# Optimization experiments

Measured on AMD Instinct MI355X. Metric: run time of the kernel, lower is better.

The kernel has to match this reference:

```python
import jax, jax.numpy as jnp
import numpy as np

N_NODES = 50000
N_EDGES = 800000
IN_CH = 64
OUT_CH = 64
EDGE_DIM = 3


def setup_inputs() -> dict:
    key = jax.random.key(0)
    k1, k2, k3, k4, k5 = jax.random.split(key, 5)
    x = jax.random.normal(k1, (N_NODES, IN_CH), dtype=jnp.float32)
    edge_index = jax.random.randint(k2, (2, N_EDGES), 0, N_NODES, dtype=jnp.int64)
    edge_attr = jax.random.normal(k3, (N_EDGES, EDGE_DIM), dtype=jnp.float32)
    # nn.Linear default init: U(-1/sqrt(fan_in), 1/sqrt(fan_in)); weight shape [out, in]
    bound = 1.0 / np.sqrt(IN_CH)
    phi_w = jax.random.uniform(k4, (OUT_CH, IN_CH), minval=-bound, maxval=bound, dtype=jnp.float32)
    psi_w = jax.random.uniform(k5, (OUT_CH, IN_CH), minval=-bound, maxval=bound, dtype=jnp.float32)
    return {"x": x, "edge_index": edge_index, "edge_attr": edge_attr, "phi_w": phi_w, "psi_w": psi_w}


def reference(x, edge_index, edge_attr, phi_w, psi_w):
    src, dst = edge_index[0], edge_index[1]
    # gather -> linear -> scale by edge-attr L2 norm
    msg = jnp.einsum('ei,oi->eo', x[src], phi_w)  # [E, out_ch]
    msg = msg * jnp.linalg.norm(edge_attr, axis=1, keepdims=True)
    # scatter-add into destination nodes
    agg = jax.ops.segment_sum(msg, dst, num_segments=x.shape[0])  # [N, out_ch]
    return jnp.einsum('ni,oi->no', x, psi_w) + agg
```

## Files before the change

kernel.cpp:

```cpp
#include <hip/hip_runtime.h>
#include <math.h>

#define NN 50000
#define NE 800000
#define CH 64
#define CSLOT 64
#define LDA 129

typedef float v4f __attribute__((ext_vector_type(4)));
typedef unsigned short u16x8 __attribute__((ext_vector_type(8)));

__device__ __forceinline__ unsigned short f2bf(float f) {
    unsigned int u = __float_as_uint(f);
    unsigned int r = (u + 0x7FFFu + ((u >> 16) & 1u)) >> 16;
    return (unsigned short)r;
}
__device__ __forceinline__ float bf2f(unsigned short h) {
    return __uint_as_float(((unsigned int)h) << 16);
}

__global__ __launch_bounds__(256) void cvt_k(const float* __restrict__ x,
                                             unsigned short* __restrict__ x16) {
    const int i = blockIdx.x * 256 + threadIdx.x;
    if (i * 8 >= NN * CH) return;
    const v4f a = *(const v4f*)(x + (size_t)i * 8);
    const v4f b = *(const v4f*)(x + (size_t)i * 8 + 4);
    u16x8 o;
    o[0] = f2bf(a.x); o[1] = f2bf(a.y); o[2] = f2bf(a.z); o[3] = f2bf(a.w);
    o[4] = f2bf(b.x); o[5] = f2bf(b.y); o[6] = f2bf(b.z); o[7] = f2bf(b.w);
    *(u16x8*)(x16 + (size_t)i * 8) = o;
}

__global__ __launch_bounds__(256) void place8x_k(const int* __restrict__ ei,
                                                 const float* __restrict__ ea,
                                                 int* __restrict__ count,
                                                 int2* __restrict__ slots) {
    const int xcd  = blockIdx.x & 7;
    const int grp  = blockIdx.x >> 3;
    const int ngrp = gridDim.x >> 3;
    const int per  = (NE + ngrp - 1) / ngrp;
    const int e0 = grp * per;
    const int e1 = (e0 + per < NE) ? e0 + per : NE;
    for (int e = e0 + threadIdx.x; e < e1; e += 256) {
        const int dst = ei[NE + e];
        if ((dst & 7) != xcd) continue;
        const int src = ei[e];
        const float a0 = ea[3 * e + 0];
        const float a1 = ea[3 * e + 1];
        const float a2 = ea[3 * e + 2];
        const float nrm = sqrtf(a0 * a0 + a1 * a1 + a2 * a2);
        const int r = atomicAdd(&count[dst], 1);
        if (r < CSLOT) {
            int2 v; v.x = src; v.y = __float_as_int(nrm);
            slots[(size_t)dst * CSLOT + r] = v;
        }
    }
}

__global__ __launch_bounds__(256) void agg8b_k(const unsigned short* __restrict__ x16,
                                               const int* __restrict__ count,
                                               const int2* __restrict__ slots,
                                               float* __restrict__ s) {
    const int c = threadIdx.x & 63;
    const int n = (int)((blockIdx.x * 256u + threadIdx.x) >> 6);
    if (n >= NN) return;
    int cnt = count[n]; if (cnt > CSLOT) cnt = CSLOT;
    const int2* sl = slots + (size_t)n * CSLOT;
    float acc0 = 0.f, acc1 = 0.f;
    int j = 0;
    for (; j + 8 <= cnt; j += 8) {
        const int2 p0 = sl[j],     p1 = sl[j + 1], p2 = sl[j + 2], p3 = sl[j + 3];
        const int2 p4 = sl[j + 4], p5 = sl[j + 5], p6 = sl[j + 6], p7 = sl[j + 7];
        const float x0 = bf2f(x16[(size_t)p0.x * CH + c]);
        const float x1 = bf2f(x16[(size_t)p1.x * CH + c]);
        const float x2 = bf2f(x16[(size_t)p2.x * CH + c]);
        const float x3 = bf2f(x16[(size_t)p3.x * CH + c]);
        const float x4 = bf2f(x16[(size_t)p4.x * CH + c]);
        const float x5 = bf2f(x16[(size_t)p5.x * CH + c]);
        const float x6 = bf2f(x16[(size_t)p6.x * CH + c]);
        const float x7 = bf2f(x16[(size_t)p7.x * CH + c]);
        acc0 = fmaf(__int_as_float(p0.y), x0, acc0);
        acc1 = fmaf(__int_as_float(p1.y), x1, acc1);
        acc0 = fmaf(__int_as_float(p2.y), x2, acc0);
        acc1 = fmaf(__int_as_float(p3.y), x3, acc1);
        acc0 = fmaf(__int_as_float(p4.y), x4, acc0);
        acc1 = fmaf(__int_as_float(p5.y), x5, acc1);
        acc0 = fmaf(__int_as_float(p6.y), x6, acc0);
        acc1 = fmaf(__int_as_float(p7.y), x7, acc1);
    }
    for (; j < cnt; ++j) {
        const int2 p = sl[j];
        acc0 = fmaf(__int_as_float(p.y), bf2f(x16[(size_t)p.x * CH + c]), acc0);
    }
    s[(size_t)n * CH + c] = acc0 + acc1;
}

__global__ __launch_bounds__(256) void scatter_r2(const float* __restrict__ x,
                                                  const int* __restrict__ ei,
                                                  const float* __restrict__ ea,
                                                  float* s) {
    const int lane = threadIdx.x & 63;
    int w = (int)((blockIdx.x * 256u + threadIdx.x) >> 6);
    const int nw = (int)((gridDim.x * 256u) >> 6);
    for (int e = w; e < NE; e += nw) {
        const int src = ei[e];
        const int dst = ei[NE + e];
        const float a0 = ea[3 * e + 0];
        const float a1 = ea[3 * e + 1];
        const float a2 = ea[3 * e + 2];
        const float nrm = sqrtf(a0 * a0 + a1 * a1 + a2 * a2);
        atomicAdd(&s[(size_t)dst * CH + lane], nrm * x[(size_t)src * CH + lane]);
    }
}

__global__ __launch_bounds__(256, 2) void out_gemm_k(const float* __restrict__ x,
                                                     const float* s,
                                                     const float* __restrict__ phi,
                                                     const float* __restrict__ psi,
                                                     float* out) {
    __shared__ float A[64][LDA];
    __shared__ float B[64][LDA];
    const int t = threadIdx.x;
    const int n0 = blockIdx.x * 64;

    for (int idx = t; idx < 64 * 16; idx += 256) {
        const int o = idx >> 4, j = idx & 15;
        v4f p = *(const v4f*)(psi + (size_t)o * CH + 4 * j);
        v4f q = *(const v4f*)(phi + (size_t)o * CH + 4 * j);
        *(v4f*)&B[o][4 * j] = p;
        *(v4f*)&B[o][64 + 4 * j] = q;
    }
    for (int idx = t; idx < 64 * 16; idx += 256) {
        const int r = idx >> 4, j = idx & 15;
        const int n = n0 + r;
        v4f xv = {0.f, 0.f, 0.f, 0.f}, sv = {0.f, 0.f, 0.f, 0.f};
        if (n < NN) {
            xv = *(const v4f*)(x + (size_t)n * CH + 4 * j);
            sv = *(const v4f*)(s + (size_t)n * CH + 4 * j);
        }
        *(v4f*)&A[r][4 * j] = xv;
        *(v4f*)&A[r][64 + 4 * j] = sv;
    }
    __syncthreads();

    const int r0 = (t >> 4) * 4;
    const int c0 = (t & 15) * 4;
    float acc[4][4] = {{0.f}};
#pragma clang loop unroll_count(2)
    for (int i = 0; i < 128; i += 4) {
        v4f a0 = *(const v4f*)&A[r0 + 0][i];
        v4f a1 = *(const v4f*)&A[r0 + 1][i];
        v4f a2 = *(const v4f*)&A[r0 + 2][i];
        v4f a3 = *(const v4f*)&A[r0 + 3][i];
        v4f b0 = *(const v4f*)&B[c0 + 0][i];
        v4f b1 = *(const v4f*)&B[c0 + 1][i];
        v4f b2 = *(const v4f*)&B[c0 + 2][i];
        v4f b3 = *(const v4f*)&B[c0 + 3][i];
#define FMA4(k, av)                                   \
        acc[k][0] = fmaf(av.x, b0.x, acc[k][0]);      \
        acc[k][0] = fmaf(av.y, b0.y, acc[k][0]);      \
        acc[k][0] = fmaf(av.z, b0.z, acc[k][0]);      \
        acc[k][0] = fmaf(av.w, b0.w, acc[k][0]);      \
        acc[k][1] = fmaf(av.x, b1.x, acc[k][1]);      \
        acc[k][1] = fmaf(av.y, b1.y, acc[k][1]);      \
        acc[k][1] = fmaf(av.z, b1.z, acc[k][1]);      \
        acc[k][1] = fmaf(av.w, b1.w, acc[k][1]);      \
        acc[k][2] = fmaf(av.x, b2.x, acc[k][2]);      \
        acc[k][2] = fmaf(av.y, b2.y, acc[k][2]);      \
        acc[k][2] = fmaf(av.z, b2.z, acc[k][2]);      \
        acc[k][2] = fmaf(av.w, b2.w, acc[k][2]);      \
        acc[k][3] = fmaf(av.x, b3.x, acc[k][3]);      \
        acc[k][3] = fmaf(av.y, b3.y, acc[k][3]);      \
        acc[k][3] = fmaf(av.z, b3.z, acc[k][3]);      \
        acc[k][3] = fmaf(av.w, b3.w, acc[k][3])
        FMA4(0, a0);
        FMA4(1, a1);
        FMA4(2, a2);
        FMA4(3, a3);
#undef FMA4
    }

#pragma unroll
    for (int k = 0; k < 4; ++k) {
        const int n = n0 + r0 + k;
        if (n < NN) {
            v4f v; v.x = acc[k][0]; v.y = acc[k][1]; v.z = acc[k][2]; v.w = acc[k][3];
            *(v4f*)(out + (size_t)n * CH + c0) = v;
        }
    }
}

extern "C" void kernel_launch(void* const* d_in, const int* in_sizes, int n_in,
                              void* d_out, int out_size, void* d_ws, size_t ws_size,
                              hipStream_t stream) {
    const float* x   = (const float*)d_in[0];
    const int*   ei  = (const int*)d_in[1];
    const float* ea  = (const float*)d_in[2];
    const float* phi = (const float*)d_in[3];
    const float* psi = (const float*)d_in[4];
    float* out = (float*)d_out;

    const int ngemm = (NN + 63) / 64;
    const int nagg  = (NN * 64 + 255) / 256;
    const int ncvt  = (NN * CH / 8 + 255) / 256;

    const size_t need = (size_t)NN * CSLOT * 8 + (size_t)NN * 4 + (size_t)NN * CH * 2;

    if (ws_size >= need) {
        int2* slots = (int2*)d_ws;
        int* count  = (int*)(slots + (size_t)NN * CSLOT);
        unsigned short* x16 = (unsigned short*)(count + NN);

        (void)hipMemsetAsync(count, 0, (size_t)NN * sizeof(int), stream);
        cvt_k<<<ncvt, 256, 0, stream>>>(x, x16);
        place8x_k<<<2048, 256, 0, stream>>>(ei, ea, count, slots);
        agg8b_k<<<nagg, 256, 0, stream>>>(x16, count, slots, out);
        out_gemm_k<<<ngemm, 256, 0, stream>>>(x, out, phi, psi, out);
    } else {
        (void)hipMemsetAsync(out, 0, (size_t)NN * CH * sizeof(float), stream);
        scatter_r2<<<4096, 256, 0, stream>>>(x, ei, ea, out);
        out_gemm_k<<<ngemm, 256, 0, stream>>>(x, out, phi, psi, out);
    }
}
```

Baseline: 186.4 us.

## Pack edge slots into 32-bit src/bf16-norm words and precompute norms in prep kernel

Fuses the x-to-bf16 conversion with a vectorized pass that precomputes per-edge L2 norms as bf16. The placement kernel then writes each slot as one 32-bit word holding a 16-bit source index and a bf16 norm, instead of an 8-byte int/float pair. It also reads edge indices with nontemporal loads. This halves slot write and read traffic in the place and aggregate kernels and drops the per-edge attribute reads from the placement loop. In exchange it adds a bf16 rounding of the norm and relies on the node count fitting in 16 bits.

```diff
diff --git a/kernel.cpp b/kernel.cpp
--- a/kernel.cpp
+++ b/kernel.cpp
@@ -9,6 +9,7 @@
 
 typedef float v4f __attribute__((ext_vector_type(4)));
 typedef unsigned short u16x8 __attribute__((ext_vector_type(8)));
+typedef unsigned short u16x4 __attribute__((ext_vector_type(4)));
 
 __device__ __forceinline__ unsigned short f2bf(float f) {
     unsigned int u = __float_as_uint(f);
@@ -19,22 +20,39 @@
     return __uint_as_float(((unsigned int)h) << 16);
 }
 
-__global__ __launch_bounds__(256) void cvt_k(const float* __restrict__ x,
-                                             unsigned short* __restrict__ x16) {
-    const int i = blockIdx.x * 256 + threadIdx.x;
-    if (i * 8 >= NN * CH) return;
-    const v4f a = *(const v4f*)(x + (size_t)i * 8);
-    const v4f b = *(const v4f*)(x + (size_t)i * 8 + 4);
-    u16x8 o;
-    o[0] = f2bf(a.x); o[1] = f2bf(a.y); o[2] = f2bf(a.z); o[3] = f2bf(a.w);
-    o[4] = f2bf(b.x); o[5] = f2bf(b.y); o[6] = f2bf(b.z); o[7] = f2bf(b.w);
-    *(u16x8*)(x16 + (size_t)i * 8) = o;
-}
-
-__global__ __launch_bounds__(256) void place8x_k(const int* __restrict__ ei,
-                                                 const float* __restrict__ ea,
-                                                 int* __restrict__ count,
-                                                 int2* __restrict__ slots) {
+#define NX8 (NN * CH / 8)
+#define NNRM (NE / 4)
+__global__ __launch_bounds__(256) void prep_k(const float* __restrict__ x,
+                                              const float* __restrict__ ea,
+                                              unsigned short* __restrict__ x16,
+                                              unsigned short* __restrict__ nrm16) {
+    const int tid = blockIdx.x * 256 + threadIdx.x;
+    if (tid < NX8) {
+        const v4f a = *(const v4f*)(x + (size_t)tid * 8);
+        const v4f b = *(const v4f*)(x + (size_t)tid * 8 + 4);
+        u16x8 o;
+        o[0] = f2bf(a.x); o[1] = f2bf(a.y); o[2] = f2bf(a.z); o[3] = f2bf(a.w);
+        o[4] = f2bf(b.x); o[5] = f2bf(b.y); o[6] = f2bf(b.z); o[7] = f2bf(b.w);
+        *(u16x8*)(x16 + (size_t)tid * 8) = o;
+    } else if (tid < NX8 + NNRM) {
+        const int e4 = (tid - NX8) * 4;
+        const float* p = ea + (size_t)e4 * 3;
+        const v4f a = *(const v4f*)(p);
+        const v4f b = *(const v4f*)(p + 4);
+        const v4f c = *(const v4f*)(p + 8);
+        u16x4 o;
+        o[0] = f2bf(sqrtf(a.x * a.x + a.y * a.y + a.z * a.z));
+        o[1] = f2bf(sqrtf(a.w * a.w + b.x * b.x + b.y * b.y));
+        o[2] = f2bf(sqrtf(b.z * b.z + b.w * b.w + c.x * c.x));
+        o[3] = f2bf(sqrtf(c.y * c.y + c.z * c.z + c.w * c.w));
+        *(u16x4*)(nrm16 + e4) = o;
+    }
+}
+
+__global__ __launch_bounds__(256) void place4_k(const int* __restrict__ ei,
+                                                const unsigned short* __restrict__ nrm16,
+                                                int* __restrict__ count,
+                                                unsigned int* __restrict__ slots) {
     const int xcd  = blockIdx.x & 7;
     const int grp  = blockIdx.x >> 3;
     const int ngrp = gridDim.x >> 3;
@@ -42,55 +60,51 @@
     const int e0 = grp * per;
     const int e1 = (e0 + per < NE) ? e0 + per : NE;
     for (int e = e0 + threadIdx.x; e < e1; e += 256) {
-        const int dst = ei[NE + e];
+        const int dst = __builtin_nontemporal_load(ei + NE + e);
         if ((dst & 7) != xcd) continue;
-        const int src = ei[e];
-        const float a0 = ea[3 * e + 0];
-        const float a1 = ea[3 * e + 1];
-        const float a2 = ea[3 * e + 2];
-        const float nrm = sqrtf(a0 * a0 + a1 * a1 + a2 * a2);
+        const int src = __builtin_nontemporal_load(ei + e);
+        const unsigned short nr = nrm16[e];
         const int r = atomicAdd(&count[dst], 1);
-        if (r < CSLOT) {
-            int2 v; v.x = src; v.y = __float_as_int(nrm);
-            slots[(size_t)dst * CSLOT + r] = v;
-        }
-    }
-}
-
-__global__ __launch_bounds__(256) void agg8b_k(const unsigned short* __restrict__ x16,
-                                               const int* __restrict__ count,
-                                               const int2* __restrict__ slots,
-                                               float* __restrict__ s) {
+        if (r < CSLOT)
+            slots[(size_t)dst * CSLOT + r] = ((unsigned int)src << 16) | nr;
+    }
+}
+
+__global__ __launch_bounds__(256) void agg4_k(const unsigned short* __restrict__ x16,
+                                              const int* __restrict__ count,
+                                              const unsigned int* __restrict__ slots,
+                                              float* __restrict__ s) {
     const int c = threadIdx.x & 63;
     const int n = (int)((blockIdx.x * 256u + threadIdx.x) >> 6);
     if (n >= NN) return;
     int cnt = count[n]; if (cnt > CSLOT) cnt = CSLOT;
-    const int2* sl = slots + (size_t)n * CSLOT;
+    const unsigned int* sl = slots + (size_t)n * CSLOT;
     float acc0 = 0.f, acc1 = 0.f;
     int j = 0;
     for (; j + 8 <= cnt; j += 8) {
-        const int2 p0 = sl[j],     p1 = sl[j + 1], p2 = sl[j + 2], p3 = sl[j + 3];
-        const int2 p4 = sl[j + 4], p5 = sl[j + 5], p6 = sl[j + 6], p7 = sl[j + 7];
-        const float x0 = bf2f(x16[(size_t)p0.x * CH + c]);
-        const float x1 = bf2f(x16[(size_t)p1.x * CH + c]);
-        const float x2 = bf2f(x16[(size_t)p2.x * CH + c]);
-        const float x3 = bf2f(x16[(size_t)p3.x * CH + c]);
-        const float x4 = bf2f(x16[(size_t)p4.x * CH + c]);
-        const float x5 = bf2f(x16[(size_t)p5.x * CH + c]);
-        const float x6 = bf2f(x16[(size_t)p6.x * CH + c]);
-        const float x7 = bf2f(x16[(size_t)p7.x * CH + c]);
-        acc0 = fmaf(__int_as_float(p0.y), x0, acc0);
-        acc1 = fmaf(__int_as_float(p1.y), x1, acc1);
-        acc0 = fmaf(__int_as_float(p2.y), x2, acc0);
-        acc1 = fmaf(__int_as_float(p3.y), x3, acc1);
-        acc0 = fmaf(__int_as_float(p4.y), x4, acc0);
-        acc1 = fmaf(__int_as_float(p5.y), x5, acc1);
-        acc0 = fmaf(__int_as_float(p6.y), x6, acc0);
-        acc1 = fmaf(__int_as_float(p7.y), x7, acc1);
+        const unsigned int p0 = sl[j],     p1 = sl[j + 1], p2 = sl[j + 2], p3 = sl[j + 3];
+        const unsigned int p4 = sl[j + 4], p5 = sl[j + 5], p6 = sl[j + 6], p7 = sl[j + 7];
+        const float x0 = bf2f(x16[(size_t)(p0 >> 16) * CH + c]);
+        const float x1 = bf2f(x16[(size_t)(p1 >> 16) * CH + c]);
+        const float x2 = bf2f(x16[(size_t)(p2 >> 16) * CH + c]);
+        const float x3 = bf2f(x16[(size_t)(p3 >> 16) * CH + c]);
+        const float x4 = bf2f(x16[(size_t)(p4 >> 16) * CH + c]);
+        const float x5 = bf2f(x16[(size_t)(p5 >> 16) * CH + c]);
+        const float x6 = bf2f(x16[(size_t)(p6 >> 16) * CH + c]);
+        const float x7 = bf2f(x16[(size_t)(p7 >> 16) * CH + c]);
+        acc0 = fmaf(bf2f((unsigned short)(p0 & 0xffff)), x0, acc0);
+        acc1 = fmaf(bf2f((unsigned short)(p1 & 0xffff)), x1, acc1);
+        acc0 = fmaf(bf2f((unsigned short)(p2 & 0xffff)), x2, acc0);
+        acc1 = fmaf(bf2f((unsigned short)(p3 & 0xffff)), x3, acc1);
+        acc0 = fmaf(bf2f((unsigned short)(p4 & 0xffff)), x4, acc0);
+        acc1 = fmaf(bf2f((unsigned short)(p5 & 0xffff)), x5, acc1);
+        acc0 = fmaf(bf2f((unsigned short)(p6 & 0xffff)), x6, acc0);
+        acc1 = fmaf(bf2f((unsigned short)(p7 & 0xffff)), x7, acc1);
     }
     for (; j < cnt; ++j) {
-        const int2 p = sl[j];
-        acc0 = fmaf(__int_as_float(p.y), bf2f(x16[(size_t)p.x * CH + c]), acc0);
+        const unsigned int p = sl[j];
+        acc0 = fmaf(bf2f((unsigned short)(p & 0xffff)),
+                    bf2f(x16[(size_t)(p >> 16) * CH + c]), acc0);
     }
     s[(size_t)n * CH + c] = acc0 + acc1;
 }
@@ -202,19 +216,21 @@
 
     const int ngemm = (NN + 63) / 64;
     const int nagg  = (NN * 64 + 255) / 256;
-    const int ncvt  = (NN * CH / 8 + 255) / 256;
-
-    const size_t need = (size_t)NN * CSLOT * 8 + (size_t)NN * 4 + (size_t)NN * CH * 2;
+    const int nprep = (NX8 + NNRM + 255) / 256;
+
+    const size_t need = (size_t)NN * CSLOT * 4 + (size_t)NN * 4
+                      + (size_t)NN * CH * 2 + (size_t)NE * 2;
 
     if (ws_size >= need) {
-        int2* slots = (int2*)d_ws;
-        int* count  = (int*)(slots + (size_t)NN * CSLOT);
+        unsigned int* slots = (unsigned int*)d_ws;
+        int* count = (int*)(slots + (size_t)NN * CSLOT);
         unsigned short* x16 = (unsigned short*)(count + NN);
+        unsigned short* nrm16 = x16 + (size_t)NN * CH;
 
         (void)hipMemsetAsync(count, 0, (size_t)NN * sizeof(int), stream);
-        cvt_k<<<ncvt, 256, 0, stream>>>(x, x16);
-        place8x_k<<<2048, 256, 0, stream>>>(ei, ea, count, slots);
-        agg8b_k<<<nagg, 256, 0, stream>>>(x16, count, slots, out);
+        prep_k<<<nprep, 256, 0, stream>>>(x, ea, x16, nrm16);
+        place4_k<<<2048, 256, 0, stream>>>(ei, nrm16, count, slots);
+        agg4_k<<<nagg, 256, 0, stream>>>(x16, count, slots, out);
         out_gemm_k<<<ngemm, 256, 0, stream>>>(x, out, phi, psi, out);
     } else {
         (void)hipMemsetAsync(out, 0, (size_t)NN * CH * sizeof(float), stream);
```

Result: no change. 188.0 us (+0.8%).
